# Performance work log

Measured on AMD Instinct MI355X. Metric: run time of the kernel, lower is better.

Reference implementation:

```python
import jax, jax.numpy as jnp
import numpy as np
from itertools import product

S0 = 384          # voxel grid size per max_data_size
N0 = 500_000      # active surface voxels
NF_IN, NF = 2, 16
EPS = 1e-4        # scn.BatchNormReLU default eps


def _make_nbr(lin, S, offs):
    # submanifold rulebook: nbr[k, i] = row of active neighbor of site i at offset k, else sentinel N
    N = len(lin)
    x = lin // (S * S); y = (lin // S) % S; z = lin % S
    nbr = np.full((len(offs), N), N, np.int32)
    for k, (dx, dy, dz) in enumerate(offs):
        nx, ny, nz = x + dx, y + dy, z + dz
        valid = (nx >= 0) & (nx < S) & (ny >= 0) & (ny < S) & (nz >= 0) & (nz < S)
        q = (nx * S + ny) * S + nz
        pos = np.minimum(np.searchsorted(lin, q), N - 1)
        nbr[k] = np.where(valid & (lin[pos] == q), pos, N).astype(np.int32)
    return nbr


def _downsample(lin, S):
    # half-resolution active sites, unpool parent map, and 2x2x2 stride-2 conv rulebook
    x = lin // (S * S); y = (lin // S) % S; z = lin % S
    Sh = S // 2
    plin = ((x // 2) * Sh + (y // 2)) * Sh + (z // 2)
    lin_h = np.unique(plin)
    parent = np.searchsorted(lin_h, plin).astype(np.int32)
    xh = lin_h // (Sh * Sh); yh = (lin_h // Sh) % Sh; zh = lin_h % Sh
    N, Nh = len(lin), len(lin_h)
    down = np.full((8, Nh), N, np.int32)
    for k, (ox, oy, oz) in enumerate(product((0, 1), repeat=3)):
        q = ((2 * xh + ox) * S + (2 * yh + oy)) * S + (2 * zh + oz)
        pos = np.minimum(np.searchsorted(lin, q), N - 1)
        down[k] = np.where(lin[pos] == q, pos, N).astype(np.int32)
    return lin_h, parent, down


def setup_inputs() -> dict:
    rng = np.random.default_rng(0)
    cand = rng.integers(0, S0 ** 3, size=int(N0 * 1.1))
    lin0 = np.unique(cand)[:N0]
    assert len(lin0) == N0
    offs27 = list(product((-1, 0, 1), repeat=3))
    nbr0 = _make_nbr(lin0, S0, offs27)
    lin1, parent01, down01 = _downsample(lin0, S0)
    nbr1 = _make_nbr(lin1, S0 // 2, offs27)
    lin2, parent12, down12 = _downsample(lin1, S0 // 2)
    nbr2 = _make_nbr(lin2, S0 // 4, offs27)

    key = jax.random.key(0)
    ks = jax.random.split(key, 16)
    n = lambda k, sh, sc: jax.random.normal(k, sh, jnp.float32) * sc
    return dict(
        feats=n(ks[0], (N0, NF_IN), 1.0),
        w_p1=n(ks[1], (27, NF_IN, NF), 1.0 / np.sqrt(27 * NF_IN)),
        blk_bn1_g=1.0 + n(ks[2], (3, NF), 0.1), blk_bn1_b=n(ks[3], (3, NF), 0.1),
        blk_w1=n(ks[4], (3, 27, NF, NF), 1.0 / np.sqrt(27 * NF)),
        blk_bn2_g=1.0 + n(ks[5], (3, NF), 0.1), blk_bn2_b=n(ks[6], (3, NF), 0.1),
        blk_w2=n(ks[7], (3, 27, NF, NF), 1.0 / np.sqrt(27 * NF)),
        down_bn_g=1.0 + n(ks[8], (2, NF), 0.1), down_bn_b=n(ks[9], (2, NF), 0.1),
        down_w=n(ks[10], (2, 8, NF, NF), 1.0 / np.sqrt(8 * NF)),
        bn3_g=1.0 + n(ks[11], (3 * NF,), 0.1), bn3_b=n(ks[12], (3 * NF,), 0.1),
        w_sdf=n(ks[13], (3 * NF, 1), 1.0 / np.sqrt(3 * NF)),
        b_sdf=jnp.zeros((1,), jnp.float32),
        nbr0=jnp.asarray(nbr0), nbr1=jnp.asarray(nbr1), nbr2=jnp.asarray(nbr2),
        down01=jnp.asarray(down01), down12=jnp.asarray(down12),
        parent01=jnp.asarray(parent01), parent12=jnp.asarray(parent12),
    )


def _sconv(x, nbr, W):
    # rulebook gather-GEMM-accumulate sparse conv.
    # x: [Nin, Cin], nbr: [K, Nout] (index Nin == inactive sentinel), W: [K, Cin, Cout]
    xp = jnp.concatenate([x, jnp.zeros((1, x.shape[1]), x.dtype)], 0)
    acc0 = jnp.zeros((nbr.shape[1], W.shape[2]), x.dtype)
    def step(acc, kw):
        idx, Wk = kw
        return acc + xp[idx] @ Wk, None
    out, _ = jax.lax.scan(step, acc0, (nbr, W))
    return out


def _bnrelu(x, g, b):
    # SCN BatchNorm: batch stats over active sites only
    m = x.mean(0); v = x.var(0)
    return jax.nn.relu((x - m) * jax.lax.rsqrt(v + EPS) * g + b)


def _res_block(x, nbr, g1, b1, w1, g2, b2, w2):
    # pre-activation residual block, identity skip (in == out channels)
    h = _sconv(_bnrelu(x, g1, b1), nbr, w1)
    h = _sconv(_bnrelu(h, g2, b2), nbr, w2)
    return x + h


def reference(feats, w_p1, blk_bn1_g, blk_bn1_b, blk_w1, blk_bn2_g, blk_bn2_b,
              blk_w2, down_bn_g, down_bn_b, down_w, bn3_g, bn3_b, w_sdf, b_sdf,
              nbr0, nbr1, nbr2, down01, down12, parent01, parent12):
    blk = lambda x, nbr, i: _res_block(x, nbr, blk_bn1_g[i], blk_bn1_b[i], blk_w1[i],
                                       blk_bn2_g[i], blk_bn2_b[i], blk_w2[i])
    x = _sconv(feats, nbr0, w_p1)                                    # p1: submanifold conv nf_in->nf
    r0 = blk(x, nbr0, 0)                                             # FCN level 0 block
    y1 = _sconv(_bnrelu(r0, down_bn_g[0], down_bn_b[0]), down01, down_w[0])  # stride-2 conv
    r1 = blk(y1, nbr1, 1)                                            # level 1 block
    z2 = _sconv(_bnrelu(r1, down_bn_g[1], down_bn_b[1]), down12, down_w[1])
    r2 = blk(z2, nbr2, 2)                                            # level 2 block
    j1 = jnp.concatenate([r1, r2[parent12]], axis=-1)                # UnPool + JoinTable -> 2*nf
    j0 = jnp.concatenate([r0, j1[parent01]], axis=-1)                # UnPool + JoinTable -> 3*nf
    h = _bnrelu(j0, bn3_g, bn3_b)                                    # p3
    return h @ w_sdf + b_sdf                                         # sdf linear, [N0, 1]
```

## Files before the change

### kernel.cpp

```cpp
#include <hip/hip_runtime.h>

#define BN_EPS 1e-4f
#define NREP 16

typedef _Float16 f16x8 __attribute__((ext_vector_type(8)));
typedef _Float16 f16x4 __attribute__((ext_vector_type(4)));
typedef _Float16 f16x2 __attribute__((ext_vector_type(2)));
typedef float f32x4 __attribute__((ext_vector_type(4)));

__global__ __launch_bounds__(256) void build_k(
    const int* __restrict__ nbr, int N, int Nin, int ngroups,
    int* __restrict__ gcnt, int* __restrict__ ent)
{
    const int wave = threadIdx.x >> 6, lane = threadIdx.x & 63;
    const int l15 = lane & 15, q = lane >> 4;

    for (int grp = blockIdx.x * 4 + wave; grp < ngroups; grp += gridDim.x * 4) {
        const int site = grp * 16 + l15;
        int v[7];
        unsigned act = 0;
#pragma unroll
        for (int p = 0; p < 7; ++p) {
            const int t = 4 * p + q;
            int idx = Nin;
            if (t < 27 && site < N) idx = nbr[(size_t)t * N + site];
            v[p] = idx;
            const unsigned long long bal = __ballot(idx < Nin);
#pragma unroll
            for (int qq = 0; qq < 4; ++qq) {
                const int tt = 4 * p + qq;
                if (tt < 27 && ((bal >> (16 * qq)) & 0xFFFFull)) act |= 1u << tt;
            }
        }
        const int cnt = __popc(act);
        if (lane == 0) gcnt[grp] = cnt;
        const int e0 = grp * 27;
#pragma unroll
        for (int p = 0; p < 7; ++p) {
            const int t = 4 * p + q;
            if (t < 27 && ((act >> t) & 1)) {
                const int e = __popc(act & ((1u << t) - 1));
                ent[(size_t)(e0 + e) * 16 + l15] = (v[p] << 5) | t;
            }
        }
    }
}

__global__ __launch_bounds__(256, 4) void conv16c_k(
    const _Float16* __restrict__ A16,
    const int* __restrict__ gcnt,
    const int* __restrict__ ent,
    const _Float16* __restrict__ WT,
    float* __restrict__ out,
    float* __restrict__ stats_out,
    int Nout, int Nin, int addSkip)
{
    __shared__ _Float16 WTs[27 * 2 * 16 * 8];
    __shared__ float TRS[4][16 * 20];
    __shared__ float RED[4][32];

    const int wave = threadIdx.x >> 6, lane = threadIdx.x & 63;
    const int l15 = lane & 15, q = lane >> 4;
    const int h = q & 1, th = q >> 1;
    const int SENT = Nin << 5;
    float* Tr = TRS[wave];

    {
        const float4* s = (const float4*)WT;
        float4* d = (float4*)WTs;
        for (int v = threadIdx.x; v < 27 * 2 * 16; v += 256) d[v] = s[v];
    }
    __syncthreads();

    const int ngroups = (Nout + 15) >> 4;
    const int stride = gridDim.x * 4;
    const int rr = lane >> 2, cc = (lane & 3) * 4;
    float sj[4] = {0.f, 0.f, 0.f, 0.f}, qj[4] = {0.f, 0.f, 0.f, 0.f};

    int grp = blockIdx.x * 4 + wave;
    int cc_cur = 0, cc_nxt = 0;
    int pe[14];
    if (grp < ngroups) {
        cc_cur = gcnt[grp];
        const int g1 = grp + stride;
        if (g1 < ngroups) cc_nxt = gcnt[g1];
        const size_t e0 = (size_t)grp * 27;
#pragma unroll
        for (int pp = 0; pp < 14; ++pp) {
            const int sidx = 2 * pp + th;
            int r = SENT;
            if (sidx < cc_cur) r = ent[(e0 + sidx) * 16 + l15];
            pe[pp] = r;
        }
    }

    while (grp < ngroups) {
        const int C = cc_cur;
        int ce[14];
#pragma unroll
        for (int pp = 0; pp < 14; ++pp) ce[pp] = pe[pp];

        const int base = grp * 16, srow = base + rr;
        float4 skip = make_float4(0.f, 0.f, 0.f, 0.f);
        if (addSkip && srow < Nout)
            skip = *(const float4*)(out + (size_t)srow * 16 + cc);

        const int gn = grp + stride;
        int cc_nn = 0;
        if (gn < ngroups) {
            const size_t e0n = (size_t)gn * 27;
#pragma unroll
            for (int pp = 0; pp < 14; ++pp) {
                const int sidx = 2 * pp + th;
                int r = SENT;
                if (sidx < cc_nxt) r = ent[(e0n + sidx) * 16 + l15];
                pe[pp] = r;
            }
            const int gnn = gn + stride;
            if (gnn < ngroups) cc_nn = gcnt[gnn];
        }

        const int np = (C + 1) >> 1;
        f32x4 acc0 = {0.f, 0.f, 0.f, 0.f}, acc1 = {0.f, 0.f, 0.f, 0.f};
#pragma unroll
        for (int pp = 0; pp < 14; ++pp) {
            if (pp < np) {
                const int raw = ce[pp];
                const int tap = raw & 31;
                f16x8 a = {};
                if (raw < SENT)
                    a = *(const f16x8*)((const char*)A16 + (raw & ~31) + h * 16);
                const f16x8 b = *(const f16x8*)(WTs + ((tap * 2 + h) * 16 + l15) * 8);
                if (pp & 1) acc1 = __builtin_amdgcn_mfma_f32_16x16x32_f16(a, b, acc1, 0, 0, 0);
                else        acc0 = __builtin_amdgcn_mfma_f32_16x16x32_f16(a, b, acc0, 0, 0, 0);
            }
        }

#pragma unroll
        for (int r = 0; r < 4; ++r)
            Tr[(q * 4 + r) * 20 + l15] = acc0[r] + acc1[r];
        float4 v4;
        v4.x = Tr[rr * 20 + cc + 0] + skip.x;
        v4.y = Tr[rr * 20 + cc + 1] + skip.y;
        v4.z = Tr[rr * 20 + cc + 2] + skip.z;
        v4.w = Tr[rr * 20 + cc + 3] + skip.w;
        if (srow < Nout) {
            *(float4*)(out + (size_t)srow * 16 + cc) = v4;
            sj[0] += v4.x; qj[0] += v4.x * v4.x;
            sj[1] += v4.y; qj[1] += v4.y * v4.y;
            sj[2] += v4.z; qj[2] += v4.z * v4.z;
            sj[3] += v4.w; qj[3] += v4.w * v4.w;
        }
        cc_cur = cc_nxt; cc_nxt = cc_nn;
        grp = gn;
    }

    if (stats_out) {
#pragma unroll
        for (int m = 4; m < 64; m <<= 1) {
#pragma unroll
            for (int j = 0; j < 4; ++j) {
                sj[j] += __shfl_xor(sj[j], m);
                qj[j] += __shfl_xor(qj[j], m);
            }
        }
        if (lane < 4) {
#pragma unroll
            for (int j = 0; j < 4; ++j) {
                RED[wave][lane * 4 + j] = sj[j];
                RED[wave][16 + lane * 4 + j] = qj[j];
            }
        }
        __syncthreads();
        if (threadIdx.x < 32) {
            const int t2 = threadIdx.x;
            float* bank = stats_out + (blockIdx.x & (NREP - 1)) * 128;
            atomicAdd(bank + (t2 < 16 ? t2 : 48 + t2),
                      RED[0][t2] + RED[1][t2] + RED[2][t2] + RED[3][t2]);
        }
    }
}

template <int K>
__global__ __launch_bounds__(256, 4) void conv16_k(
    const _Float16* __restrict__ A16, const int* __restrict__ nbr,
    const _Float16* __restrict__ WB, float* __restrict__ out,
    float* __restrict__ stats_out, int Nout, int Nin, int addSkip)
{
    constexpr int PAIRS = (K + 1) / 2;
    const int wave = threadIdx.x >> 6, lane = threadIdx.x & 63;
    const int l15 = lane & 15, q = lane >> 4;
    const int h = q & 1, th = q >> 1;

    f16x8 bfr[PAIRS];
#pragma unroll
    for (int p = 0; p < PAIRS; ++p)
        bfr[p] = *(const f16x8*)(WB + ((size_t)p * 64 + lane) * 8);

    const int ngroups = (Nout + 15) >> 4;
    float s = 0.f, ss = 0.f;

    for (int grp = blockIdx.x * 4 + wave; grp < ngroups; grp += gridDim.x * 4) {
        const int base = grp * 16;
        const int site = min(base + l15, Nout - 1);
        f32x4 acc0 = {0.f, 0.f, 0.f, 0.f}, acc1 = {0.f, 0.f, 0.f, 0.f};
#pragma unroll
        for (int p = 0; p < PAIRS; ++p) {
            const int t = 2 * p + ((2 * p + 1 < K) ? th : 0);
            const int idx = nbr[(size_t)t * Nout + site];
            f16x8 a = {};
            if (idx < Nin)
                a = *(const f16x8*)(A16 + (size_t)idx * 16 + h * 8);
            if (p & 1) acc1 = __builtin_amdgcn_mfma_f32_16x16x32_f16(a, bfr[p], acc1, 0, 0, 0);
            else       acc0 = __builtin_amdgcn_mfma_f32_16x16x32_f16(a, bfr[p], acc0, 0, 0, 0);
        }
#pragma unroll
        for (int r = 0; r < 4; ++r) {
            const int row = base + q * 4 + r;
            float v = acc0[r] + acc1[r];
            if (row < Nout) {
                float* op = out + (size_t)row * 16 + l15;
                if (addSkip) v += *op;
                *op = v;
                s += v; ss += v * v;
            }
        }
    }

    if (stats_out) {
        s  += __shfl_xor(s, 16);  s  += __shfl_xor(s, 32);
        ss += __shfl_xor(ss, 16); ss += __shfl_xor(ss, 32);
        __shared__ float red[4][32];
        if (lane < 16) { red[wave][l15] = s; red[wave][16 + l15] = ss; }
        __syncthreads();
        if (threadIdx.x < 32) {
            const int t2 = threadIdx.x;
            float* bank = stats_out + (blockIdx.x & (NREP - 1)) * 128;
            atomicAdd(bank + (t2 < 16 ? t2 : 48 + t2),
                      red[0][t2] + red[1][t2] + red[2][t2] + red[3][t2]);
        }
    }
}

__global__ __launch_bounds__(256, 4) void convp1_k(
    const _Float16* __restrict__ F16,
    const int* __restrict__ nbr,
    const _Float16* __restrict__ WB,
    float* __restrict__ out, float* __restrict__ stats_out, int N)
{
    const int wave = threadIdx.x >> 6, lane = threadIdx.x & 63;
    const int l15 = lane & 15, q = lane >> 4;

    f16x8 b0 = *(const f16x8*)(WB + (size_t)lane * 8);
    f16x8 b1 = *(const f16x8*)(WB + ((size_t)64 + lane) * 8);

    const int ngroups = (N + 15) >> 4;
    float s = 0.f, ss = 0.f;

    for (int grp = blockIdx.x * 4 + wave; grp < ngroups; grp += gridDim.x * 4) {
        const int base = grp * 16;
        const int site = min(base + l15, N - 1);
        int tid[8];
#pragma unroll
        for (int u = 0; u < 8; ++u) {
            const int t = (u < 4) ? (q * 4 + u) : (16 + q * 4 + (u - 4));
            tid[u] = (t < 27) ? nbr[(size_t)t * N + site] : N;
        }
        f32x4 acc = {0.f, 0.f, 0.f, 0.f};
#pragma unroll
        for (int mf = 0; mf < 2; ++mf) {
            f16x8 a;
#pragma unroll
            for (int jt = 0; jt < 4; ++jt) {
                const int idx = tid[mf * 4 + jt];
                f16x2 f = {};
                if (idx < N) f = *(const f16x2*)(F16 + (size_t)idx * 2);
                a[jt * 2] = f.x; a[jt * 2 + 1] = f.y;
            }
            acc = __builtin_amdgcn_mfma_f32_16x16x32_f16(a, mf ? b1 : b0, acc, 0, 0, 0);
        }
#pragma unroll
        for (int r = 0; r < 4; ++r) {
            const int row = base + q * 4 + r;
            const float v = acc[r];
            if (row < N) {
                out[(size_t)row * 16 + l15] = v;
                s += v; ss += v * v;
            }
        }
    }

    s  += __shfl_xor(s, 16);  s  += __shfl_xor(s, 32);
    ss += __shfl_xor(ss, 16); ss += __shfl_xor(ss, 32);
    __shared__ float red[4][32];
    if (lane < 16) { red[wave][l15] = s; red[wave][16 + l15] = ss; }
    __syncthreads();
    if (threadIdx.x < 32) {
        const int t2 = threadIdx.x;
        float* bank = stats_out + (blockIdx.x & (NREP - 1)) * 128;
        atomicAdd(bank + (t2 < 16 ? t2 : 48 + t2),
                  red[0][t2] + red[1][t2] + red[2][t2] + red[3][t2]);
    }
}

__global__ void pack_k(const float* __restrict__ w_p1, const float* __restrict__ w1,
                       const float* __restrict__ w2, const float* __restrict__ dw,
                       _Float16* __restrict__ WBp1, _Float16* __restrict__ WT27,
                       _Float16* __restrict__ WB8)
{
    const int b = blockIdx.x;
    if (b == 0) {
        for (int v = threadIdx.x; v < 2 * 64 * 8; v += 256) {
            const int mf = v >> 9, lane = (v >> 3) & 63, j = v & 7;
            const int qq = lane >> 4, n = lane & 15;
            const int kg = mf * 32 + qq * 8 + j;
            const int t = kg >> 1, cin = kg & 1;
            WBp1[v] = (t < 27) ? (_Float16)w_p1[t * 32 + cin * 16 + n] : (_Float16)0.f;
        }
    } else if (b <= 6) {
        const int ti = b - 1, lvl = ti >> 1;
        const float* src = ((ti & 1) ? w2 : w1) + lvl * 6912;
        _Float16* dst = WT27 + (size_t)ti * 6912;
        for (int v = threadIdx.x; v < 6912; v += 256) {
            const int j = v & 7, n = (v >> 3) & 15, hh = (v >> 7) & 1, t = v >> 8;
            dst[v] = (_Float16)src[t * 256 + (hh * 8 + j) * 16 + n];
        }
    } else {
        const int ti = b - 7;
        const float* src = dw + ti * 2048;
        _Float16* dst = WB8 + (size_t)ti * (4 * 64 * 8);
        for (int v = threadIdx.x; v < 4 * 64 * 8; v += 256) {
            const int p = v >> 9, lane = (v >> 3) & 63, j = v & 7;
            const int qq = lane >> 4, n = lane & 15;
            const int t = 2 * p + (qq >> 1);
            const int cin = (qq & 1) * 8 + j;
            dst[v] = (_Float16)src[t * 256 + cin * 16 + n];
        }
    }
}

__global__ __launch_bounds__(256) void apply16_k(
    const float* __restrict__ x, const float* __restrict__ stats,
    const float* __restrict__ g, const float* __restrict__ b,
    _Float16* __restrict__ A16, int N, float invN)
{
    __shared__ float sbl[2][16];
    if (threadIdx.x < 16) {
        const int c = threadIdx.x;
        float su = 0.f, sq = 0.f;
#pragma unroll
        for (int rep = 0; rep < NREP; ++rep) {
            su += stats[rep * 128 + c];
            sq += stats[rep * 128 + 64 + c];
        }
        const float mean = su * invN;
        const float var = sq * invN - mean * mean;
        const float sc = g[c] * rsqrtf(var + BN_EPS);
        sbl[0][c] = sc;
        sbl[1][c] = fmaf(-mean, sc, b[c]);
    }
    __syncthreads();

    const int t = blockIdx.x * 256 + threadIdx.x;
    if (t >= (N + 1) * 4) return;
    const int n = t >> 2, c = (t & 3) * 4;
    f16x4 r;
    if (n == N) {
        r[0] = r[1] = r[2] = r[3] = (_Float16)0.f;
    } else {
        const float4 v = *(const float4*)(x + (size_t)n * 16 + c);
        float vv[4] = {v.x, v.y, v.z, v.w};
#pragma unroll
        for (int i = 0; i < 4; ++i)
            r[i] = (_Float16)fmaxf(fmaf(vv[i], sbl[0][c + i], sbl[1][c + i]), 0.f);
    }
    *(f16x4*)(A16 + (size_t)n * 16 + c) = r;
}

__global__ void f16cvt_k(const float* __restrict__ f, _Float16* __restrict__ F16, int N)
{
    const int t = blockIdx.x * 256 + threadIdx.x;
    if (t > N) return;
    f16x2 r;
    if (t == N) { r[0] = r[1] = (_Float16)0.f; }
    else { const float2 v = *(const float2*)(f + (size_t)t * 2); r[0] = (_Float16)v.x; r[1] = (_Float16)v.y; }
    *(f16x2*)(F16 + (size_t)t * 2) = r;
}

__global__ void fin_k(float* __restrict__ stats, const float* __restrict__ g,
                      const float* __restrict__ b, float* __restrict__ sb,
                      int C, float invN)
{
    const int c = threadIdx.x;
    if (c < C) {
        float su = 0.f, sq = 0.f;
#pragma unroll
        for (int rep = 0; rep < NREP; ++rep) {
            su += stats[rep * 128 + c];
            sq += stats[rep * 128 + 64 + c];
        }
        const float mean = su * invN;
        const float var = sq * invN - mean * mean;
        const float s = g[c] * rsqrtf(var + BN_EPS);
        sb[c] = s;
        sb[64 + c] = fmaf(-mean, s, b[c]);
    }
}

__device__ __forceinline__ float wred(float v) {
#pragma unroll
    for (int off = 32; off > 0; off >>= 1) v += __shfl_xor(v, off);
    return v;
}

__global__ __launch_bounds__(256) void gstats_k(
    const float* __restrict__ R0, const float* __restrict__ R1,
    const float* __restrict__ R2, const int* __restrict__ p01,
    const int* __restrict__ p12, float* __restrict__ stats, int N0)
{
    float s[48], q[48];
#pragma unroll
    for (int c = 0; c < 48; ++c) { s[c] = 0.f; q[c] = 0.f; }

    for (int n = blockIdx.x * blockDim.x + threadIdx.x; n < N0;
         n += gridDim.x * blockDim.x) {
        const int i1 = p01[n];
        const int i2 = p12[i1];
        const float4* a0 = (const float4*)(R0 + (size_t)n * 16);
        const float4* a1 = (const float4*)(R1 + (size_t)i1 * 16);
        const float4* a2 = (const float4*)(R2 + (size_t)i2 * 16);
#pragma unroll
        for (int j = 0; j < 4; ++j) {
            const float4 v = a0[j]; const int c = 4 * j;
            s[c] += v.x; q[c] += v.x * v.x; s[c+1] += v.y; q[c+1] += v.y * v.y;
            s[c+2] += v.z; q[c+2] += v.z * v.z; s[c+3] += v.w; q[c+3] += v.w * v.w;
        }
#pragma unroll
        for (int j = 0; j < 4; ++j) {
            const float4 v = a1[j]; const int c = 16 + 4 * j;
            s[c] += v.x; q[c] += v.x * v.x; s[c+1] += v.y; q[c+1] += v.y * v.y;
            s[c+2] += v.z; q[c+2] += v.z * v.z; s[c+3] += v.w; q[c+3] += v.w * v.w;
        }
#pragma unroll
        for (int j = 0; j < 4; ++j) {
            const float4 v = a2[j]; const int c = 32 + 4 * j;
            s[c] += v.x; q[c] += v.x * v.x; s[c+1] += v.y; q[c+1] += v.y * v.y;
            s[c+2] += v.z; q[c+2] += v.z * v.z; s[c+3] += v.w; q[c+3] += v.w * v.w;
        }
    }

    __shared__ float red[4][96];
    const int wave = threadIdx.x >> 6, lane = threadIdx.x & 63;
#pragma unroll
    for (int c = 0; c < 48; ++c) {
        const float ss = wred(s[c]);
        const float qq = wred(q[c]);
        if (lane == 0) { red[wave][c] = ss; red[wave][48 + c] = qq; }
    }
    __syncthreads();
    const int t = threadIdx.x;
    if (t < 96) {
        float* bank = stats + (blockIdx.x & (NREP - 1)) * 128;
        const float v = red[0][t] + red[1][t] + red[2][t] + red[3][t];
        atomicAdd(bank + (t < 48 ? t : 64 + (t - 48)), v);
    }
}

__global__ __launch_bounds__(256) void out_k(
    const float* __restrict__ R0, const float* __restrict__ R1,
    const float* __restrict__ R2, const int* __restrict__ p01,
    const int* __restrict__ p12, const float* __restrict__ sb,
    const float* __restrict__ wsdf, const float* __restrict__ bsdf,
    float* __restrict__ out, int N0)
{
    const int n = blockIdx.x * 256 + threadIdx.x;
    if (n >= N0) return;
    const int i1 = p01[n];
    const int i2 = p12[i1];
    float acc = bsdf[0];
    const float4* a0 = (const float4*)(R0 + (size_t)n * 16);
    const float4* a1 = (const float4*)(R1 + (size_t)i1 * 16);
    const float4* a2 = (const float4*)(R2 + (size_t)i2 * 16);
#pragma unroll
    for (int j = 0; j < 4; ++j) {
        const float4 v = a0[j]; const int c = 4 * j;
        acc += fmaxf(fmaf(v.x, sb[c+0], sb[64+c+0]), 0.f) * wsdf[c+0];
        acc += fmaxf(fmaf(v.y, sb[c+1], sb[64+c+1]), 0.f) * wsdf[c+1];
        acc += fmaxf(fmaf(v.z, sb[c+2], sb[64+c+2]), 0.f) * wsdf[c+2];
        acc += fmaxf(fmaf(v.w, sb[c+3], sb[64+c+3]), 0.f) * wsdf[c+3];
    }
#pragma unroll
    for (int j = 0; j < 4; ++j) {
        const float4 v = a1[j]; const int c = 16 + 4 * j;
        acc += fmaxf(fmaf(v.x, sb[c+0], sb[64+c+0]), 0.f) * wsdf[c+0];
        acc += fmaxf(fmaf(v.y, sb[c+1], sb[64+c+1]), 0.f) * wsdf[c+1];
        acc += fmaxf(fmaf(v.z, sb[c+2], sb[64+c+2]), 0.f) * wsdf[c+2];
        acc += fmaxf(fmaf(v.w, sb[c+3], sb[64+c+3]), 0.f) * wsdf[c+3];
    }
#pragma unroll
    for (int j = 0; j < 4; ++j) {
        const float4 v = a2[j]; const int c = 32 + 4 * j;
        acc += fmaxf(fmaf(v.x, sb[c+0], sb[64+c+0]), 0.f) * wsdf[c+0];
        acc += fmaxf(fmaf(v.y, sb[c+1], sb[64+c+1]), 0.f) * wsdf[c+1];
        acc += fmaxf(fmaf(v.z, sb[c+2], sb[64+c+2]), 0.f) * wsdf[c+2];
        acc += fmaxf(fmaf(v.w, sb[c+3], sb[64+c+3]), 0.f) * wsdf[c+3];
    }
    out[n] = acc;
}

extern "C" void kernel_launch(void* const* d_in, const int* in_sizes, int n_in,
                              void* d_out, int out_size, void* d_ws, size_t ws_size,
                              hipStream_t stream)
{
    const float* feats = (const float*)d_in[0];
    const float* w_p1  = (const float*)d_in[1];
    const float* bn1g  = (const float*)d_in[2];
    const float* bn1b  = (const float*)d_in[3];
    const float* w1    = (const float*)d_in[4];
    const float* bn2g  = (const float*)d_in[5];
    const float* bn2b  = (const float*)d_in[6];
    const float* w2    = (const float*)d_in[7];
    const float* dbng  = (const float*)d_in[8];
    const float* dbnb  = (const float*)d_in[9];
    const float* dw    = (const float*)d_in[10];
    const float* bn3g  = (const float*)d_in[11];
    const float* bn3b  = (const float*)d_in[12];
    const float* wsdf  = (const float*)d_in[13];
    const float* bsdf  = (const float*)d_in[14];
    const int* nbr0    = (const int*)d_in[15];
    const int* nbr1    = (const int*)d_in[16];
    const int* nbr2    = (const int*)d_in[17];
    const int* down01  = (const int*)d_in[18];
    const int* down12  = (const int*)d_in[19];
    const int* p01     = (const int*)d_in[20];
    const int* p12     = (const int*)d_in[21];

    const int N0 = in_sizes[0] / 2;
    const int N1 = in_sizes[18] / 8;
    const int N2 = in_sizes[19] / 8;
    const int ng0 = (N0 + 15) / 16, ng1 = (N1 + 15) / 16, ng2 = (N2 + 15) / 16;
    const int maxe = ng0 * 27 + 64;

    char* wp = (char*)d_ws;
    auto alloc = [&](size_t bytes) { char* r = wp; wp += (bytes + 255) & ~(size_t)255; return r; };
    float* T  = (float*)alloc((size_t)N0 * 16 * 4);
    float* R0 = (float*)alloc((size_t)N0 * 16 * 4);
    float* R1 = (float*)alloc((size_t)N1 * 16 * 4);
    float* R2 = (float*)alloc((size_t)N2 * 16 * 4);
    float* st = (float*)alloc(9 * NREP * 128 * 4);
    float* sb = (float*)alloc(128 * 4);
    _Float16* A16  = (_Float16*)alloc((size_t)(N0 + 1) * 16 * 2);
    _Float16* F16  = (_Float16*)alloc((size_t)(N0 + 1) * 2 * 2);
    _Float16* WBp1 = (_Float16*)alloc(2 * 64 * 8 * 2);
    _Float16* WT27 = (_Float16*)alloc(6 * 6912 * 2);
    _Float16* WB8  = (_Float16*)alloc(2 * 4 * 64 * 8 * 2);
    int* gcnt = (int*)alloc((size_t)ng0 * 4);
    int* ent  = (int*)alloc((size_t)maxe * 16 * 4);

    hipMemsetAsync(st, 0, 9 * NREP * 128 * sizeof(float), stream);

    const dim3 B(256);
    auto cgrid = [](int n) {
        const int g = (((n + 15) / 16) + 3) / 4;
        return dim3((unsigned)(g < 2048 ? g : 2048));
    };
    auto agrid = [](int n) { return dim3((unsigned)(((n + 1) * 4 + 255) / 256)); };
    auto lgrid = [](int n) { return dim3((unsigned)((n + 255) / 256)); };
    const float i0 = 1.0f / N0, i1 = 1.0f / N1, i2 = 1.0f / N2;
    auto S = [&](int i) { return st + i * NREP * 128; };
    auto WT = [&](int i) { return WT27 + (size_t)i * 6912; };
    auto W8 = [&](int i) { return WB8 + (size_t)i * (4 * 64 * 8); };

    pack_k<<<9, B, 0, stream>>>(w_p1, w1, w2, dw, WBp1, WT27, WB8);
    f16cvt_k<<<lgrid(N0 + 1), B, 0, stream>>>(feats, F16, N0);

    build_k<<<cgrid(N0), B, 0, stream>>>(nbr0, N0, N0, ng0, gcnt, ent);
    convp1_k<<<cgrid(N0), B, 0, stream>>>(F16, nbr0, WBp1, R0, S(0), N0);
    apply16_k<<<agrid(N0), B, 0, stream>>>(R0, S(0), bn1g, bn1b, A16, N0, i0);
    conv16c_k<<<cgrid(N0), B, 0, stream>>>(A16, gcnt, ent, WT(0), T, S(1), N0, N0, 0);
    apply16_k<<<agrid(N0), B, 0, stream>>>(T, S(1), bn2g, bn2b, A16, N0, i0);
    conv16c_k<<<cgrid(N0), B, 0, stream>>>(A16, gcnt, ent, WT(1), R0, S(2), N0, N0, 1);
    apply16_k<<<agrid(N0), B, 0, stream>>>(R0, S(2), dbng, dbnb, A16, N0, i0);
    conv16_k<8><<<cgrid(N1), B, 0, stream>>>(A16, down01, W8(0), R1, S(3), N1, N0, 0);

    build_k<<<cgrid(N1), B, 0, stream>>>(nbr1, N1, N1, ng1, gcnt, ent);
    apply16_k<<<agrid(N1), B, 0, stream>>>(R1, S(3), bn1g + 16, bn1b + 16, A16, N1, i1);
    conv16c_k<<<cgrid(N1), B, 0, stream>>>(A16, gcnt, ent, WT(2), T, S(4), N1, N1, 0);
    apply16_k<<<agrid(N1), B, 0, stream>>>(T, S(4), bn2g + 16, bn2b + 16, A16, N1, i1);
    conv16c_k<<<cgrid(N1), B, 0, stream>>>(A16, gcnt, ent, WT(3), R1, S(5), N1, N1, 1);
    apply16_k<<<agrid(N1), B, 0, stream>>>(R1, S(5), dbng + 16, dbnb + 16, A16, N1, i1);
    conv16_k<8><<<cgrid(N2), B, 0, stream>>>(A16, down12, W8(1), R2, S(6), N2, N1, 0);

    build_k<<<cgrid(N2), B, 0, stream>>>(nbr2, N2, N2, ng2, gcnt, ent);
    apply16_k<<<agrid(N2), B, 0, stream>>>(R2, S(6), bn1g + 32, bn1b + 32, A16, N2, i2);
    conv16c_k<<<cgrid(N2), B, 0, stream>>>(A16, gcnt, ent, WT(4), T, S(7), N2, N2, 0);
    apply16_k<<<agrid(N2), B, 0, stream>>>(T, S(7), bn2g + 32, bn2b + 32, A16, N2, i2);
    conv16c_k<<<cgrid(N2), B, 0, stream>>>(A16, gcnt, ent, WT(5), R2, nullptr, N2, N2, 1);

    gstats_k<<<512, B, 0, stream>>>(R0, R1, R2, p01, p12, S(8), N0);
    fin_k<<<1, 64, 0, stream>>>(S(8), bn3g, bn3b, sb, 48, i0);
    out_k<<<lgrid(N0), B, 0, stream>>>(R0, R1, R2, p01, p12, sb, wsdf, bsdf,
                                       (float*)d_out, N0);
}
```

Before: 659.1 us.

## Fuse BatchNorm-ReLU and fp16 conversion into the convolution gather loads

Removes the separate apply16 and f16cvt kernels. Each convolution kernel now folds the per-channel BN statistics into a scale and bias at block start. It then applies scale, bias, ReLU and the fp16 cast to every gathered fp32 neighbor row just before the MFMA. This drops several launches and the round trip through the fp16 activation buffer. In exchange, each gather reads fp32 instead of fp16, doubling gathered bytes, and the BN/ReLU math is redone for each of the up to 27 taps that reuse a row.

```diff
diff --git a/kernel.cpp b/kernel.cpp
--- a/kernel.cpp
+++ b/kernel.cpp
@@ -4,7 +4,6 @@
 #define NREP 16
 
 typedef _Float16 f16x8 __attribute__((ext_vector_type(8)));
-typedef _Float16 f16x4 __attribute__((ext_vector_type(4)));
 typedef _Float16 f16x2 __attribute__((ext_vector_type(2)));
 typedef float f32x4 __attribute__((ext_vector_type(4)));
 
@@ -47,10 +46,14 @@
 }
 
 __global__ __launch_bounds__(256, 4) void conv16c_k(
-    const _Float16* __restrict__ A16,
+    const float* __restrict__ act,
     const int* __restrict__ gcnt,
     const int* __restrict__ ent,
     const _Float16* __restrict__ WT,
+    const float* __restrict__ g,
+    const float* __restrict__ b,
+    const float* __restrict__ stats_in,
+    float invN,
     float* __restrict__ out,
     float* __restrict__ stats_out,
     int Nout, int Nin, int addSkip)
@@ -58,6 +61,7 @@
     __shared__ _Float16 WTs[27 * 2 * 16 * 8];
     __shared__ float TRS[4][16 * 20];
     __shared__ float RED[4][32];
+    __shared__ float sbl[2][16];
 
     const int wave = threadIdx.x >> 6, lane = threadIdx.x & 63;
     const int l15 = lane & 15, q = lane >> 4;
@@ -69,8 +73,29 @@
         const float4* s = (const float4*)WT;
         float4* d = (float4*)WTs;
         for (int v = threadIdx.x; v < 27 * 2 * 16; v += 256) d[v] = s[v];
+        if (threadIdx.x < 16) {
+            const int c = threadIdx.x;
+            float su = 0.f, sq = 0.f;
+#pragma unroll
+            for (int rep = 0; rep < NREP; ++rep) {
+                su += stats_in[rep * 128 + c];
+                sq += stats_in[rep * 128 + 64 + c];
+            }
+            const float mean = su * invN;
+            const float var = sq * invN - mean * mean;
+            const float sc = g[c] * rsqrtf(var + BN_EPS);
+            sbl[0][c] = sc;
+            sbl[1][c] = fmaf(-mean, sc, b[c]);
+        }
     }
     __syncthreads();
+
+    float scv[8], biv[8];
+#pragma unroll
+    for (int j = 0; j < 8; ++j) {
+        scv[j] = sbl[0][h * 8 + j];
+        biv[j] = sbl[1][h * 8 + j];
+    }
 
     const int ngroups = (Nout + 15) >> 4;
     const int stride = gridDim.x * 4;
@@ -128,11 +153,19 @@
                 const int raw = ce[pp];
                 const int tap = raw & 31;
                 f16x8 a = {};
-                if (raw < SENT)
-                    a = *(const f16x8*)((const char*)A16 + (raw & ~31) + h * 16);
-                const f16x8 b = *(const f16x8*)(WTs + ((tap * 2 + h) * 16 + l15) * 8);
-                if (pp & 1) acc1 = __builtin_amdgcn_mfma_f32_16x16x32_f16(a, b, acc1, 0, 0, 0);
-                else        acc0 = __builtin_amdgcn_mfma_f32_16x16x32_f16(a, b, acc0, 0, 0, 0);
+                if (raw < SENT) {
+                    const float* rp = act + ((size_t)(raw >> 5) * 16 + h * 8);
+                    const float4 x0 = ((const float4*)rp)[0];
+                    const float4 x1 = ((const float4*)rp)[1];
+                    const float y[8] = {x0.x, x0.y, x0.z, x0.w,
+                                        x1.x, x1.y, x1.z, x1.w};
+#pragma unroll
+                    for (int j = 0; j < 8; ++j)
+                        a[j] = (_Float16)fmaxf(fmaf(y[j], scv[j], biv[j]), 0.f);
+                }
+                const f16x8 bb = *(const f16x8*)(WTs + ((tap * 2 + h) * 16 + l15) * 8);
+                if (pp & 1) acc1 = __builtin_amdgcn_mfma_f32_16x16x32_f16(a, bb, acc1, 0, 0, 0);
+                else        acc0 = __builtin_amdgcn_mfma_f32_16x16x32_f16(a, bb, acc0, 0, 0, 0);
             }
         }
 
@@ -183,14 +216,41 @@
 
 template <int K>
 __global__ __launch_bounds__(256, 4) void conv16_k(
-    const _Float16* __restrict__ A16, const int* __restrict__ nbr,
-    const _Float16* __restrict__ WB, float* __restrict__ out,
-    float* __restrict__ stats_out, int Nout, int Nin, int addSkip)
+    const float* __restrict__ act, const int* __restrict__ nbr,
+    const _Float16* __restrict__ WB,
+    const float* __restrict__ g, const float* __restrict__ b,
+    const float* __restrict__ stats_in, float invN,
+    float* __restrict__ out, float* __restrict__ stats_out,
+    int Nout, int Nin, int addSkip)
 {
     constexpr int PAIRS = (K + 1) / 2;
+    __shared__ float sbl[2][16];
     const int wave = threadIdx.x >> 6, lane = threadIdx.x & 63;
     const int l15 = lane & 15, q = lane >> 4;
     const int h = q & 1, th = q >> 1;
+
+    if (threadIdx.x < 16) {
+        const int c = threadIdx.x;
+        float su = 0.f, sq = 0.f;
+#pragma unroll
+        for (int rep = 0; rep < NREP; ++rep) {
+            su += stats_in[rep * 128 + c];
+            sq += stats_in[rep * 128 + 64 + c];
+        }
+        const float mean = su * invN;
+        const float var = sq * invN - mean * mean;
+        const float sc = g[c] * rsqrtf(var + BN_EPS);
+        sbl[0][c] = sc;
+        sbl[1][c] = fmaf(-mean, sc, b[c]);
+    }
+    __syncthreads();
+
+    float scv[8], biv[8];
+#pragma unroll
+    for (int j = 0; j < 8; ++j) {
+        scv[j] = sbl[0][h * 8 + j];
+        biv[j] = sbl[1][h * 8 + j];
+    }
 
     f16x8 bfr[PAIRS];
 #pragma unroll
@@ -209,8 +269,16 @@
             const int t = 2 * p + ((2 * p + 1 < K) ? th : 0);
             const int idx = nbr[(size_t)t * Nout + site];
             f16x8 a = {};
-            if (idx < Nin)
-                a = *(const f16x8*)(A16 + (size_t)idx * 16 + h * 8);
+            if (idx < Nin) {
+                const float* rp = act + ((size_t)idx * 16 + h * 8);
+                const float4 x0 = ((const float4*)rp)[0];
+                const float4 x1 = ((const float4*)rp)[1];
+                const float y[8] = {x0.x, x0.y, x0.z, x0.w,
+                                    x1.x, x1.y, x1.z, x1.w};
+#pragma unroll
+                for (int j = 0; j < 8; ++j)
+                    a[j] = (_Float16)fmaxf(fmaf(y[j], scv[j], biv[j]), 0.f);
+            }
             if (p & 1) acc1 = __builtin_amdgcn_mfma_f32_16x16x32_f16(a, bfr[p], acc1, 0, 0, 0);
             else       acc0 = __builtin_amdgcn_mfma_f32_16x16x32_f16(a, bfr[p], acc0, 0, 0, 0);
         }
@@ -243,7 +311,7 @@
 }
 
 __global__ __launch_bounds__(256, 4) void convp1_k(
-    const _Float16* __restrict__ F16,
+    const float* __restrict__ feats,
     const int* __restrict__ nbr,
     const _Float16* __restrict__ WB,
     float* __restrict__ out, float* __restrict__ stats_out, int N)
@@ -273,9 +341,9 @@
 #pragma unroll
             for (int jt = 0; jt < 4; ++jt) {
                 const int idx = tid[mf * 4 + jt];
-                f16x2 f = {};
-                if (idx < N) f = *(const f16x2*)(F16 + (size_t)idx * 2);
-                a[jt * 2] = f.x; a[jt * 2 + 1] = f.y;
+                float2 f = make_float2(0.f, 0.f);
+                if (idx < N) f = *(const float2*)(feats + (size_t)idx * 2);
+                a[jt * 2] = (_Float16)f.x; a[jt * 2 + 1] = (_Float16)f.y;
             }
             acc = __builtin_amdgcn_mfma_f32_16x16x32_f16(a, mf ? b1 : b0, acc, 0, 0, 0);
         }
@@ -337,54 +405,6 @@
             dst[v] = (_Float16)src[t * 256 + cin * 16 + n];
         }
     }
-}
-
-__global__ __launch_bounds__(256) void apply16_k(
-    const float* __restrict__ x, const float* __restrict__ stats,
-    const float* __restrict__ g, const float* __restrict__ b,
-    _Float16* __restrict__ A16, int N, float invN)
-{
-    __shared__ float sbl[2][16];
-    if (threadIdx.x < 16) {
-        const int c = threadIdx.x;
-        float su = 0.f, sq = 0.f;
-#pragma unroll
-        for (int rep = 0; rep < NREP; ++rep) {
-            su += stats[rep * 128 + c];
-            sq += stats[rep * 128 + 64 + c];
-        }
-        const float mean = su * invN;
-        const float var = sq * invN - mean * mean;
-        const float sc = g[c] * rsqrtf(var + BN_EPS);
-        sbl[0][c] = sc;
-        sbl[1][c] = fmaf(-mean, sc, b[c]);
-    }
-    __syncthreads();
-
-    const int t = blockIdx.x * 256 + threadIdx.x;
-    if (t >= (N + 1) * 4) return;
-    const int n = t >> 2, c = (t & 3) * 4;
-    f16x4 r;
-    if (n == N) {
-        r[0] = r[1] = r[2] = r[3] = (_Float16)0.f;
-    } else {
-        const float4 v = *(const float4*)(x + (size_t)n * 16 + c);
-        float vv[4] = {v.x, v.y, v.z, v.w};
-#pragma unroll
-        for (int i = 0; i < 4; ++i)
-            r[i] = (_Float16)fmaxf(fmaf(vv[i], sbl[0][c + i], sbl[1][c + i]), 0.f);
-    }
-    *(f16x4*)(A16 + (size_t)n * 16 + c) = r;
-}
-
-__global__ void f16cvt_k(const float* __restrict__ f, _Float16* __restrict__ F16, int N)
-{
-    const int t = blockIdx.x * 256 + threadIdx.x;
-    if (t > N) return;
-    f16x2 r;
-    if (t == N) { r[0] = r[1] = (_Float16)0.f; }
-    else { const float2 v = *(const float2*)(f + (size_t)t * 2); r[0] = (_Float16)v.x; r[1] = (_Float16)v.y; }
-    *(f16x2*)(F16 + (size_t)t * 2) = r;
 }
 
 __global__ void fin_k(float* __restrict__ stats, const float* __restrict__ g,
@@ -549,8 +569,6 @@
     float* R2 = (float*)alloc((size_t)N2 * 16 * 4);
     float* st = (float*)alloc(9 * NREP * 128 * 4);
     float* sb = (float*)alloc(128 * 4);
-    _Float16* A16  = (_Float16*)alloc((size_t)(N0 + 1) * 16 * 2);
-    _Float16* F16  = (_Float16*)alloc((size_t)(N0 + 1) * 2 * 2);
     _Float16* WBp1 = (_Float16*)alloc(2 * 64 * 8 * 2);
     _Float16* WT27 = (_Float16*)alloc(6 * 6912 * 2);
     _Float16* WB8  = (_Float16*)alloc(2 * 4 * 64 * 8 * 2);
@@ -564,7 +582,6 @@
         const int g = (((n + 15) / 16) + 3) / 4;
         return dim3((unsigned)(g < 2048 ? g : 2048));
     };
-    auto agrid = [](int n) { return dim3((unsigned)(((n + 1) * 4 + 255) / 256)); };
     auto lgrid = [](int n) { return dim3((unsigned)((n + 255) / 256)); };
     const float i0 = 1.0f / N0, i1 = 1.0f / N1, i2 = 1.0f / N2;
     auto S = [&](int i) { return st + i * NREP * 128; };
@@ -572,30 +589,29 @@
     auto W8 = [&](int i) { return WB8 + (size_t)i * (4 * 64 * 8); };
 
     pack_k<<<9, B, 0, stream>>>(w_p1, w1, w2, dw, WBp1, WT27, WB8);
-    f16cvt_k<<<lgrid(N0 + 1), B, 0, stream>>>(feats, F16, N0);
 
     build_k<<<cgrid(N0), B, 0, stream>>>(nbr0, N0, N0, ng0, gcnt, ent);
-    convp1_k<<<cgrid(N0), B, 0, stream>>>(F16, nbr0, WBp1, R0, S(0), N0);
-    apply16_k<<<agrid(N0), B, 0, stream>>>(R0, S(0), bn1g, bn1b, A16, N0, i0);
-    conv16c_k<<<cgrid(N0), B, 0, stream>>>(A16, gcnt, ent, WT(0), T, S(1), N0, N0, 0);
-    apply16_k<<<agrid(N0), B, 0, stream>>>(T, S(1), bn2g, bn2b, A16, N0, i0);
-    conv16c_k<<<cgrid(N0), B, 0, stream>>>(A16, gcnt, ent, WT(1), R0, S(2), N0, N0, 1);
-    apply16_k<<<agrid(N0), B, 0, stream>>>(R0, S(2), dbng, dbnb, A16, N0, i0);
-    conv16_k<8><<<cgrid(N1), B, 0, stream>>>(A16, down01, W8(0), R1, S(3), N1, N0, 0);
+    convp1_k<<<cgrid(N0), B, 0, stream>>>(feats, nbr0, WBp1, R0, S(0), N0);
+    conv16c_k<<<cgrid(N0), B, 0, stream>>>(R0, gcnt, ent, WT(0), bn1g, bn1b,
+                                           S(0), i0, T, S(1), N0, N0, 0);
+    conv16c_k<<<cgrid(N0), B, 0, stream>>>(T, gcnt, ent, WT(1), bn2g, bn2b,
+                                           S(1), i0, R0, S(2), N0, N0, 1);
+    conv16_k<8><<<cgrid(N1), B, 0, stream>>>(R0, down01, W8(0), dbng, dbnb,
+                                             S(2), i0, R1, S(3), N1, N0, 0);
 
     build_k<<<cgrid(N1), B, 0, stream>>>(nbr1, N1, N1, ng1, gcnt, ent);
-    apply16_k<<<agrid(N1), B, 0, stream>>>(R1, S(3), bn1g + 16, bn1b + 16, A16, N1, i1);
-    conv16c_k<<<cgrid(N1), B, 0, stream>>>(A16, gcnt, ent, WT(2), T, S(4), N1, N1, 0);
-    apply16_k<<<agrid(N1), B, 0, stream>>>(T, S(4), bn2g + 16, bn2b + 16, A16, N1, i1);
-    conv16c_k<<<cgrid(N1), B, 0, stream>>>(A16, gcnt, ent, WT(3), R1, S(5), N1, N1, 1);
-    apply16_k<<<agrid(N1), B, 0, stream>>>(R1, S(5), dbng + 16, dbnb + 16, A16, N1, i1);
-    conv16_k<8><<<cgrid(N2), B, 0, stream>>>(A16, down12, W8(1), R2, S(6), N2, N1, 0);
+    conv16c_k<<<cgrid(N1), B, 0, stream>>>(R1, gcnt, ent, WT(2), bn1g + 16, bn1b + 16,
+                                           S(3), i1, T, S(4), N1, N1, 0);
+    conv16c_k<<<cgrid(N1), B, 0, stream>>>(T, gcnt, ent, WT(3), bn2g + 16, bn2b + 16,
+                                           S(4), i1, R1, S(5), N1, N1, 1);
+    conv16_k<8><<<cgrid(N2), B, 0, stream>>>(R1, down12, W8(1), dbng + 16, dbnb + 16,
+                                             S(5), i1, R2, S(6), N2, N1, 0);
 
     build_k<<<cgrid(N2), B, 0, stream>>>(nbr2, N2, N2, ng2, gcnt, ent);
-    apply16_k<<<agrid(N2), B, 0, stream>>>(R2, S(6), bn1g + 32, bn1b + 32, A16, N2, i2);
-    conv16c_k<<<cgrid(N2), B, 0, stream>>>(A16, gcnt, ent, WT(4), T, S(7), N2, N2, 0);
-    apply16_k<<<agrid(N2), B, 0, stream>>>(T, S(7), bn2g + 32, bn2b + 32, A16, N2, i2);
-    conv16c_k<<<cgrid(N2), B, 0, stream>>>(A16, gcnt, ent, WT(5), R2, nullptr, N2, N2, 1);
+    conv16c_k<<<cgrid(N2), B, 0, stream>>>(R2, gcnt, ent, WT(4), bn1g + 32, bn1b + 32,
+                                           S(6), i2, T, S(7), N2, N2, 0);
+    conv16c_k<<<cgrid(N2), B, 0, stream>>>(T, gcnt, ent, WT(5), bn2g + 32, bn2b + 32,
+                                           S(7), i2, R2, nullptr, N2, N2, 1);
 
     gstats_k<<<512, B, 0, stream>>>(R0, R1, R2, p01, p12, S(8), N0);
     fin_k<<<1, 64, 0, stream>>>(S(8), bn3g, bn3b, sb, 48, i0);
```

New measurement: 660.8 us. About the same (+0.3%).
